# Kernel optimization log

Measured on AMD Instinct MI355X. Metric: run time of the kernel, lower is better.

The kernel has to match this reference:

```python
import jax, jax.numpy as jnp
import numpy as np

B, C, H, I = 32, 8, 512, 512


def act(x):
    # CustomActivation == hardtanh: (|x+1| - |x-1|) / 2
    return (jnp.abs(x + 1.0) - jnp.abs(x - 1.0)) * 0.5


def setup_inputs() -> dict:
    key = jax.random.key(0)
    ks = jax.random.split(key, 12)
    inp = jax.random.normal(ks[0], (B, C, H, I), dtype=jnp.float32)
    p_mask = jax.random.normal(ks[1], (H, I), dtype=jnp.float32)
    # Wp: tril(randn) with diagonal filled to 1 (matches __init__ + the no_grad
    # tril/clamp projection in forward, which is a no-op right after init).
    Wp = jnp.tril(jax.random.normal(ks[2], (H, H), dtype=jnp.float32))
    Wp = Wp - jnp.diag(jnp.diag(Wp)) + jnp.eye(H, dtype=jnp.float32)
    Wp_diag = jnp.ones((H,), dtype=jnp.float32)
    Wzp = jax.random.normal(ks[3], (H, H), dtype=jnp.float32)
    s = 1.0 / np.sqrt(I)
    def lin(k):
        kw, kb = jax.random.split(k)
        W = jax.random.uniform(kw, (I, I), jnp.float32, -s, s)
        b = jax.random.uniform(kb, (I,), jnp.float32, -s, s)
        return W, b
    p_lin_w, p_lin_b = lin(ks[4])
    z_lin_w, z_lin_b = lin(ks[5])
    fc1_w, fc1_b = lin(ks[6])
    fc2_w, fc2_b = lin(ks[7])
    return {
        'input': inp, 'p_mask': p_mask, 'Wp': Wp, 'Wp_diag': Wp_diag, 'Wzp': Wzp,
        'p_lin_w': p_lin_w, 'p_lin_b': p_lin_b,
        'z_lin_w': z_lin_w, 'z_lin_b': z_lin_b,
        'fc1_w': fc1_w, 'fc1_b': fc1_b, 'fc2_w': fc2_w, 'fc2_b': fc2_b,
    }


def reference(input, p_mask, Wp, Wp_diag, Wzp,
              p_lin_w, p_lin_b, z_lin_w, z_lin_b,
              fc1_w, fc1_b, fc2_w, fc2_b):
    x = input * (1.0 / 5000.0)                      # [B,C,H,I]
    p_set = x * act(p_mask)                         # split_input, broadcast over B,C
    Wp_eff = Wp + jnp.diag(Wp_diag)                 # [H,H]
    # per-channel Wp @ p_set[c], batched over B and C in one GEMM
    tp = jnp.einsum('hk,bcki->bchi', Wp_eff, p_set)
    tp = act(act(tp) @ p_lin_w.T + p_lin_b)         # p_output_layer
    tz = jnp.einsum('hk,bchi->bchi', Wzp, tp)       # wait-free channel-batched GEMM
    tz = act(act(tz) @ z_lin_w.T + z_lin_b)         # z_output_layer
    # sum over in_channel (out_channel==1 so broadcast-accumulate == sum)
    combined = tp.sum(axis=1) + tz.sum(axis=1) + x[:, 0]  # [B,H,I]
    out = jax.nn.relu(combined @ fc1_w.T + fc1_b)
    out = out @ fc2_w.T + fc2_b
    return out
```

## Files before the change

kernel.cpp:

```cpp
#include <hip/hip_runtime.h>

namespace {

constexpr int Bn = 32, Cn = 8, Hn = 512, In = 512;
constexpr size_t HI = (size_t)Hn * In;
constexpr float SC = 1.0f / 5000.0f;

using s16x8 = __attribute__((ext_vector_type(8))) short;
using f32x4 = __attribute__((ext_vector_type(4))) float;

__device__ __forceinline__ float actf(float x) {
    return fminf(1.0f, fmaxf(-1.0f, x));
}

__device__ __forceinline__ unsigned short f2bf(float f) {
    unsigned u = __builtin_bit_cast(unsigned, f);
    u += 0x7FFFu + ((u >> 16) & 1u);
    return (unsigned short)(u >> 16);
}
__device__ __forceinline__ float bf2f(unsigned short h) {
    return __builtin_bit_cast(float, (unsigned)h << 16);
}

__device__ __forceinline__ void async16(const void* g, void* l) {
    __builtin_amdgcn_global_load_lds(
        (const __attribute__((address_space(1))) unsigned*)g,
        (__attribute__((address_space(3))) unsigned*)l, 16, 0, 0);
}

#define CFENCE asm volatile("" ::: "memory")
#define BAR do { CFENCE; __builtin_amdgcn_s_barrier(); CFENCE; } while (0)

template<int EPI, bool PCOL, bool TRI>
__global__ __launch_bounds__(512, 2) void gemm256_8p(
    const unsigned short* __restrict__ A,
    const unsigned short* __restrict__ Bt,
    const float* __restrict__ bias,
    const float* __restrict__ zrow,
    unsigned short* __restrict__ out0,
    unsigned short* __restrict__ out1,
    size_t sB, size_t sC)
{
    __shared__ __align__(16) char lds[131072];
    char* daA = lds;
    char* dbA = lds + 32768;
    char* daB = lds + 65536;
    char* dbB = lds + 98304;

    const int tid = threadIdx.x;
    const int lane = tid & 63, l15 = lane & 15, kq = lane >> 4;
    const int wid = tid >> 6, wm = wid >> 2, wn = wid & 3;

    const int bid = blockIdx.x;
    int rt, ct; size_t zb;
    if (PCOL) {
        const int p = ((bid >> 5) << 3) | (bid & 7);
        const int q = (bid >> 3) & 3;
        zb = (size_t)p; rt = q >> 1; ct = q & 1;
    } else {
        const int p = ((bid >> 4) << 3) | (bid & 7);
        const int q = (bid >> 3) & 1;
        zb = 0; rt = p; ct = q;
    }

    const char* Ab = (const char*)A + (size_t)rt * 256 * 1024;
    const char* Bb = (const char*)(Bt + zb * sB) + (size_t)ct * 256 * 1024;

    const int nkt = TRI ? (rt + 1) * 4 : 8;
    const int nit = nkt >> 1;

    const int srow8 = tid >> 3;
    const int csw   = ((tid & 7) ^ (srow8 & 7)) << 4;

    auto stageH = [&](const char* src, int kt, int half, char* dstTile) {
        const char* s = src + ((size_t)half * 128 + srow8) * 1024 + kt * 128 + csw;
        char* d = dstTile + half * 16384 + tid * 16;
        async16(s,             d);
        async16(s + 64 * 1024, d + 8192);
    };

    const int kx0 = ((kq    ) ^ (l15 & 7)) << 4;
    const int kx1 = ((kq + 4) ^ (l15 & 7)) << 4;

    auto rdA4 = [&](const char* tile, int mlo, s16x8 a[2][4]) {
        #pragma unroll
        for (int i = 0; i < 4; ++i) {
            const int row = wm * 128 + (mlo + i) * 16 + l15;
            a[0][i] = *(const s16x8*)(tile + row * 128 + kx0);
            a[1][i] = *(const s16x8*)(tile + row * 128 + kx1);
        }
    };
    auto rdB2 = [&](const char* tile, int nlo, s16x8 b[2][2]) {
        #pragma unroll
        for (int j = 0; j < 2; ++j) {
            const int row = wn * 64 + (nlo + j) * 16 + l15;
            b[0][j] = *(const s16x8*)(tile + row * 128 + kx0);
            b[1][j] = *(const s16x8*)(tile + row * 128 + kx1);
        }
    };

    f32x4 acc[8][4] = {};

    auto QMM = [&](s16x8 a[2][4], s16x8 b[2][2], int mlo, int nlo) {
        __builtin_amdgcn_s_setprio(1);
        #pragma unroll
        for (int kk = 0; kk < 2; ++kk)
            #pragma unroll
            for (int i = 0; i < 4; ++i)
                #pragma unroll
                for (int j = 0; j < 2; ++j)
                    acc[mlo + i][nlo + j] = __builtin_amdgcn_mfma_f32_16x16x32_bf16(
                        a[kk][i], b[kk][j], acc[mlo + i][nlo + j], 0, 0, 0);
        __builtin_amdgcn_s_setprio(0);
    };

    stageH(Bb, 0, 0, daB); stageH(Bb, 0, 1, daB);
    stageH(Ab, 0, 0, daA); stageH(Ab, 0, 1, daA);
    stageH(Bb, 1, 0, dbB); stageH(Bb, 1, 1, dbB);
    asm volatile("s_waitcnt vmcnt(4)" ::: "memory");
    BAR;

    #pragma unroll 1
    for (int t = 0; t < nit; ++t) {
        const int j = 2 * t;
        const bool more = (t + 1 < nit);
        s16x8 a03[2][4], a47[2][4], b01[2][2], b23[2][2];

        rdA4(daA, 0, a03); rdB2(daB, 0, b01);
        stageH(Ab, j + 1, 0, dbA);
        BAR; QMM(a03, b01, 0, 0); BAR;
        rdB2(daB, 2, b23);
        stageH(Ab, j + 1, 1, dbA);
        BAR; QMM(a03, b23, 0, 2); BAR;
        rdA4(daA, 4, a47);
        if (more) stageH(Bb, j + 2, 0, daB);
        BAR; QMM(a47, b23, 4, 2); BAR;
        if (more) stageH(Bb, j + 2, 1, daB);
        BAR; QMM(a47, b01, 4, 0);
        if (more) asm volatile("s_waitcnt vmcnt(4)" ::: "memory");
        else      asm volatile("s_waitcnt vmcnt(0)" ::: "memory");
        BAR;

        rdA4(dbA, 0, a03); rdB2(dbB, 0, b01);
        if (more) stageH(Ab, j + 2, 0, daA);
        BAR; QMM(a03, b01, 0, 0); BAR;
        rdB2(dbB, 2, b23);
        if (more) stageH(Ab, j + 2, 1, daA);
        BAR; QMM(a03, b23, 0, 2); BAR;
        rdA4(dbA, 4, a47);
        if (more) stageH(Bb, j + 3, 0, dbB);
        BAR; QMM(a47, b23, 4, 2); BAR;
        if (more) stageH(Bb, j + 3, 1, dbB);
        BAR; QMM(a47, b01, 4, 0);
        if (more) { asm volatile("s_waitcnt vmcnt(4)" ::: "memory"); BAR; }
        else BAR;
    }

    const int rbase = rt * 256 + wm * 128 + kq * 4;
    const int cb    = ct * 256 + wn * 64 + l15;
    #pragma unroll
    for (int mi = 0; mi < 8; ++mi) {
        #pragma unroll
        for (int n = 0; n < 4; ++n) {
            const int c = cb + n * 16;
            const float bs = (EPI == 0) ? 0.0f : bias[c];
            #pragma unroll
            for (int jj = 0; jj < 4; ++jj) {
                const size_t r = (size_t)rbase + mi * 16 + jj;
                const size_t idx = zb * sC + r * 512 + c;
                float v = acc[mi][n][jj];
                if (EPI == 0) {
                    out0[idx] = f2bf(actf(v));
                } else if (EPI == 1) {
                    float tp = actf(v + bs);
                    out0[idx] = f2bf(tp);
                    out1[idx] = f2bf(actf(zrow[r & 511] * tp));
                } else {
                    out0[idx] = f2bf(actf(v + bs));
                }
            }
        }
    }
}

template<int EPI>
__global__ __launch_bounds__(256, 3) void mfma_gemm128(
    const unsigned short* __restrict__ A,
    const unsigned short* __restrict__ Bt,
    const float* __restrict__ bias,
    unsigned short* __restrict__ out0,
    float* __restrict__ outf)
{
    __shared__ __align__(16) char lds[2][16384];

    const int tid  = threadIdx.x;
    const int wid  = tid >> 6, lane = tid & 63;
    const int wr   = wid >> 1, wc = wid & 1;
    const int l15  = lane & 15, kq = lane >> 4;

    const int bid = blockIdx.x;
    const int p = ((bid >> 5) << 3) | (bid & 7);
    const int q = (bid >> 3) & 3;
    const int rt = p, ct = q;

    const char* Ab = (const char*)A + (size_t)rt * 131072;
    const char* Bb = (const char*)Bt + (size_t)ct * 131072;

    f32x4 acc[4][4] = {};

    const int o0  = tid * 16;
    const int r0s = o0 >> 6;
    const int c0s = o0 & 63;
    const int csw = c0s ^ (((r0s >> 1) & 3) << 4);

    auto stage = [&](char* buf, int k0b) {
        async16(Ab + (size_t)r0s * 1024 + k0b + csw,        buf + wid * 1024);
        async16(Ab + (size_t)(64 + r0s) * 1024 + k0b + csw, buf + 4096 + wid * 1024);
        async16(Bb + (size_t)r0s * 1024 + k0b + csw,        buf + 8192 + wid * 1024);
        async16(Bb + (size_t)(64 + r0s) * 1024 + k0b + csw, buf + 12288 + wid * 1024);
    };
    auto compute = [&](const char* buf) {
        s16x8 a[4], b[4];
        const int kx = kq * 16 ^ (((l15 >> 1) & 3) << 4);
        const int ar = wr * 64 + l15;
        const int br = wc * 64 + l15;
        #pragma unroll
        for (int m = 0; m < 4; ++m)
            a[m] = *(const s16x8*)(buf + (size_t)(ar + m * 16) * 64 + kx);
        #pragma unroll
        for (int n = 0; n < 4; ++n)
            b[n] = *(const s16x8*)(buf + 8192 + (size_t)(br + n * 16) * 64 + kx);
        #pragma unroll
        for (int m = 0; m < 4; ++m)
            #pragma unroll
            for (int n = 0; n < 4; ++n)
                acc[m][n] = __builtin_amdgcn_mfma_f32_16x16x32_bf16(a[m], b[n], acc[m][n], 0, 0, 0);
    };

    stage(lds[0], 0);
    stage(lds[1], 64);

    #pragma unroll 1
    for (int ks = 0; ks < 16; ks += 2) {
        const bool more = (ks + 2 < 16);
        asm volatile("s_waitcnt vmcnt(4)" ::: "memory");
        BAR;
        compute(lds[0]);
        BAR;
        if (more) stage(lds[0], (ks + 2) * 64);
        if (more) asm volatile("s_waitcnt vmcnt(4)" ::: "memory");
        else      asm volatile("s_waitcnt vmcnt(0)" ::: "memory");
        BAR;
        compute(lds[1]);
        BAR;
        if (more) stage(lds[1], (ks + 3) * 64);
    }

    const int cb = ct * 128 + wc * 64 + l15;
    const int rb = rt * 128 + wr * 64 + (kq << 2);
    #pragma unroll
    for (int m = 0; m < 4; ++m)
        #pragma unroll
        for (int n = 0; n < 4; ++n) {
            const int c = cb + n * 16;
            #pragma unroll
            for (int j = 0; j < 4; ++j) {
                const int r = rb + m * 16 + j;
                const size_t idx = (size_t)r * 512 + c;
                float v = acc[m][n][j] + bias[c];
                if (EPI == 3) out0[idx] = f2bf(fmaxf(v, 0.0f));
                else          outf[idx] = v;
            }
        }
}

__global__ __launch_bounds__(256) void reduce_both(
    const unsigned short* __restrict__ tp,
    const unsigned short* __restrict__ tz,
    const float* __restrict__ x0,
    unsigned short* __restrict__ comb)
{
    size_t idx = (size_t)blockIdx.x * 256 + threadIdx.x;
    size_t b = idx >> 16;
    size_t p = (idx & 65535) * 4;
    float4 xv = *(const float4*)&x0[(b * Cn) * HI + p];
    float s0 = xv.x * SC, s1 = xv.y * SC, s2 = xv.z * SC, s3 = xv.w * SC;
    #pragma unroll
    for (int c = 0; c < Cn; ++c) {
        size_t q = (b * Cn + c) * HI + p;
        ushort4 a = *(const ushort4*)&tp[q];
        ushort4 d = *(const ushort4*)&tz[q];
        s0 += bf2f(a.x) + bf2f(d.x);
        s1 += bf2f(a.y) + bf2f(d.y);
        s2 += bf2f(a.z) + bf2f(d.z);
        s3 += bf2f(a.w) + bf2f(d.w);
    }
    ushort4 o;
    o.x = f2bf(s0); o.y = f2bf(s1); o.z = f2bf(s2); o.w = f2bf(s3);
    *(ushort4*)&comb[b * HI + p] = o;
}

__global__ __launch_bounds__(256) void transpose_mask(
    const float* __restrict__ x, const float* __restrict__ mask,
    unsigned short* __restrict__ xst)
{
    __shared__ float t[64][65];
    const int bc = blockIdx.z;
    const int i0 = blockIdx.x * 64, k0 = blockIdx.y * 64;
    const int r4 = threadIdx.x >> 6, cc = threadIdx.x & 63;
    const float* xp = x + (size_t)bc * HI;
    #pragma unroll
    for (int it = 0; it < 16; ++it) {
        int kl = it * 4 + r4;
        size_t g = (size_t)(k0 + kl) * In + i0 + cc;
        t[kl][cc] = xp[g] * (actf(mask[g]) * SC);
    }
    __syncthreads();
    unsigned short* op = xst + (size_t)bc * HI;
    #pragma unroll
    for (int it = 0; it < 16; ++it) {
        int il = it * 4 + r4;
        op[(size_t)(i0 + il) * Hn + k0 + cc] = f2bf(t[cc][il]);
    }
}

__global__ __launch_bounds__(256) void prep_wpe_bf(
    const float* __restrict__ Wp, const float* __restrict__ Wpd,
    unsigned short* __restrict__ o)
{
    int idx = blockIdx.x * 256 + threadIdx.x;
    int i = idx >> 9, j = idx & 511;
    o[idx] = f2bf(Wp[idx] + (i == j ? Wpd[i] : 0.0f));
}

__global__ __launch_bounds__(256) void conv_bf(
    const float* __restrict__ s, unsigned short* __restrict__ o)
{
    int idx = blockIdx.x * 256 + threadIdx.x;
    o[idx] = f2bf(s[idx]);
}

__global__ __launch_bounds__(64) void rowsum(
    const float* __restrict__ W, float* __restrict__ zr)
{
    int h = blockIdx.x, l = threadIdx.x;
    float s = 0.0f;
    for (int k = l; k < Hn; k += 64) s += W[h * Hn + k];
    #pragma unroll
    for (int off = 32; off; off >>= 1) s += __shfl_down(s, off, 64);
    if (!l) zr[h] = s;
}

}

extern "C" void kernel_launch(void* const* d_in, const int* in_sizes, int n_in,
                              void* d_out, int out_size, void* d_ws, size_t ws_size,
                              hipStream_t stream)
{
    const float* input  = (const float*)d_in[0];
    const float* p_mask = (const float*)d_in[1];
    const float* Wp     = (const float*)d_in[2];
    const float* Wpd    = (const float*)d_in[3];
    const float* Wzp    = (const float*)d_in[4];
    const float* plw    = (const float*)d_in[5];
    const float* plb    = (const float*)d_in[6];
    const float* zlw    = (const float*)d_in[7];
    const float* zlb    = (const float*)d_in[8];
    const float* f1w    = (const float*)d_in[9];
    const float* f1b    = (const float*)d_in[10];
    const float* f2w    = (const float*)d_in[11];
    const float* f2b    = (const float*)d_in[12];

    constexpr size_t WB = 512 * 512 * 2;
    char* w = (char*)d_ws;
    auto alloc = [&](size_t bytes) { char* p = w; w += (bytes + 255) & ~255ull; return p; };

    unsigned short* Wpeb  = (unsigned short*)alloc(WB);
    unsigned short* plwb  = (unsigned short*)alloc(WB);
    unsigned short* zlwb  = (unsigned short*)alloc(WB);
    unsigned short* f1wb  = (unsigned short*)alloc(WB);
    unsigned short* f2wb  = (unsigned short*)alloc(WB);
    float*          zrw   = (float*)alloc(512 * 4);
    unsigned short* combb = (unsigned short*)alloc((size_t)Bn * HI * 2);
    unsigned short* out1  = (unsigned short*)alloc((size_t)Bn * HI * 2);

    size_t fixedB = (size_t)(w - (char*)d_ws);
    int chunk = 32;
    while (chunk > 1 &&
           fixedB + 4ull * (size_t)chunk * Cn * HI * 2 + 4096 > ws_size)
        chunk >>= 1;
    const size_t CB = (size_t)chunk * Cn * HI * 2;
    unsigned short* xst   = (unsigned short*)alloc(CB);
    unsigned short* tpact = (unsigned short*)alloc(CB);
    unsigned short* tpb   = (unsigned short*)alloc(CB);
    unsigned short* tzin  = (unsigned short*)alloc(CB);
    unsigned short* tzb   = xst;

    prep_wpe_bf<<<512 * 512 / 256, 256, 0, stream>>>(Wp, Wpd, Wpeb);
    conv_bf<<<1024, 256, 0, stream>>>(plw, plwb);
    conv_bf<<<1024, 256, 0, stream>>>(zlw, zlwb);
    conv_bf<<<1024, 256, 0, stream>>>(f1w, f1wb);
    conv_bf<<<1024, 256, 0, stream>>>(f2w, f2wb);
    rowsum<<<512, 64, 0, stream>>>(Wzp, zrw);

    for (int b0 = 0; b0 < Bn; b0 += chunk) {
        const int nc = chunk * Cn;
        const float* inp_c = input + (size_t)b0 * Cn * HI;

        transpose_mask<<<dim3(8, 8, nc), 256, 0, stream>>>(inp_c, p_mask, xst);
        gemm256_8p<0, true, true><<<nc * 4, 512, 0, stream>>>(
            Wpeb, xst, nullptr, nullptr, tpact, nullptr, HI, HI);
        gemm256_8p<1, false, false><<<nc * 4, 512, 0, stream>>>(
            tpact, plwb, plb, zrw, tpb, tzin, 0, 0);
        gemm256_8p<2, false, false><<<nc * 4, 512, 0, stream>>>(
            tzin, zlwb, zlb, nullptr, tzb, nullptr, 0, 0);
        reduce_both<<<chunk * 256, 256, 0, stream>>>(
            tpb, tzb, inp_c, combb + (size_t)b0 * HI);
    }

    mfma_gemm128<3><<<512, 256, 0, stream>>>(combb, f1wb, f1b, out1, nullptr);
    mfma_gemm128<4><<<512, 256, 0, stream>>>(out1, f2wb, f2b, nullptr, (float*)d_out);
}
```

Before: 489.5 us.

## Vectorize memory-bound helper kernels, fuse weight conversions, reorder triangular tiles

The reduce kernel now handles 8 elements per thread with 16-byte loads and stores, and its grid is halved to match. The transpose/mask kernel reads inputs as float4 and writes ushort4. The four weight bf16 conversions are merged into a single vectorized launch. In the triangular GEMM, the row-tile order is flipped so the heavier lower row tile is scheduled first, which should even out load imbalance. Each change is meant to cut memory instruction count or launch overhead. The transpose now does strided LDS reads with column access, which could raise bank conflicts.

Result: no change. 489.2 us, median of 2 (-0.1%).

```diff
diff --git a/kernel.cpp b/kernel.cpp
--- a/kernel.cpp
+++ b/kernel.cpp
@@ -7,6 +7,7 @@
 constexpr float SC = 1.0f / 5000.0f;
 
 using s16x8 = __attribute__((ext_vector_type(8))) short;
+using u16x8 = __attribute__((ext_vector_type(8))) unsigned short;
 using f32x4 = __attribute__((ext_vector_type(4))) float;
 
 __device__ __forceinline__ float actf(float x) {
@@ -56,7 +57,7 @@
     if (PCOL) {
         const int p = ((bid >> 5) << 3) | (bid & 7);
         const int q = (bid >> 3) & 3;
-        zb = (size_t)p; rt = q >> 1; ct = q & 1;
+        zb = (size_t)p; rt = 1 - (q >> 1); ct = q & 1;
     } else {
         const int p = ((bid >> 4) << 3) | (bid & 7);
         const int q = (bid >> 3) & 1;
@@ -281,23 +282,24 @@
     unsigned short* __restrict__ comb)
 {
     size_t idx = (size_t)blockIdx.x * 256 + threadIdx.x;
-    size_t b = idx >> 16;
-    size_t p = (idx & 65535) * 4;
-    float4 xv = *(const float4*)&x0[(b * Cn) * HI + p];
-    float s0 = xv.x * SC, s1 = xv.y * SC, s2 = xv.z * SC, s3 = xv.w * SC;
+    size_t b = idx >> 15;
+    size_t p = (idx & 32767) * 8;
+    float4 xa = *(const float4*)&x0[(b * Cn) * HI + p];
+    float4 xb = *(const float4*)&x0[(b * Cn) * HI + p + 4];
+    float s[8] = { xa.x * SC, xa.y * SC, xa.z * SC, xa.w * SC,
+                   xb.x * SC, xb.y * SC, xb.z * SC, xb.w * SC };
     #pragma unroll
     for (int c = 0; c < Cn; ++c) {
         size_t q = (b * Cn + c) * HI + p;
-        ushort4 a = *(const ushort4*)&tp[q];
-        ushort4 d = *(const ushort4*)&tz[q];
-        s0 += bf2f(a.x) + bf2f(d.x);
-        s1 += bf2f(a.y) + bf2f(d.y);
-        s2 += bf2f(a.z) + bf2f(d.z);
-        s3 += bf2f(a.w) + bf2f(d.w);
-    }
-    ushort4 o;
-    o.x = f2bf(s0); o.y = f2bf(s1); o.z = f2bf(s2); o.w = f2bf(s3);
-    *(ushort4*)&comb[b * HI + p] = o;
+        u16x8 a = *(const u16x8*)&tp[q];
+        u16x8 d = *(const u16x8*)&tz[q];
+        #pragma unroll
+        for (int j = 0; j < 8; ++j) s[j] += bf2f(a[j]) + bf2f(d[j]);
+    }
+    u16x8 o;
+    #pragma unroll
+    for (int j = 0; j < 8; ++j) o[j] = f2bf(s[j]);
+    *(u16x8*)&comb[b * HI + p] = o;
 }
 
 __global__ __launch_bounds__(256) void transpose_mask(
@@ -307,20 +309,31 @@
     __shared__ float t[64][65];
     const int bc = blockIdx.z;
     const int i0 = blockIdx.x * 64, k0 = blockIdx.y * 64;
-    const int r4 = threadIdx.x >> 6, cc = threadIdx.x & 63;
+    const int r16 = threadIdx.x >> 4;
+    const int c4  = (threadIdx.x & 15) * 4;
     const float* xp = x + (size_t)bc * HI;
     #pragma unroll
-    for (int it = 0; it < 16; ++it) {
-        int kl = it * 4 + r4;
-        size_t g = (size_t)(k0 + kl) * In + i0 + cc;
-        t[kl][cc] = xp[g] * (actf(mask[g]) * SC);
+    for (int ps = 0; ps < 4; ++ps) {
+        const int kl = ps * 16 + r16;
+        const size_t g = (size_t)(k0 + kl) * In + i0 + c4;
+        float4 xv = *(const float4*)&xp[g];
+        float4 mv = *(const float4*)&mask[g];
+        t[kl][c4 + 0] = xv.x * (actf(mv.x) * SC);
+        t[kl][c4 + 1] = xv.y * (actf(mv.y) * SC);
+        t[kl][c4 + 2] = xv.z * (actf(mv.z) * SC);
+        t[kl][c4 + 3] = xv.w * (actf(mv.w) * SC);
     }
     __syncthreads();
     unsigned short* op = xst + (size_t)bc * HI;
     #pragma unroll
-    for (int it = 0; it < 16; ++it) {
-        int il = it * 4 + r4;
-        op[(size_t)(i0 + il) * Hn + k0 + cc] = f2bf(t[cc][il]);
+    for (int ps = 0; ps < 4; ++ps) {
+        const int il = ps * 16 + r16;
+        ushort4 o;
+        o.x = f2bf(t[c4 + 0][il]);
+        o.y = f2bf(t[c4 + 1][il]);
+        o.z = f2bf(t[c4 + 2][il]);
+        o.w = f2bf(t[c4 + 3][il]);
+        *(ushort4*)&op[(size_t)(i0 + il) * Hn + k0 + c4] = o;
     }
 }
 
@@ -333,11 +346,20 @@
     o[idx] = f2bf(Wp[idx] + (i == j ? Wpd[i] : 0.0f));
 }
 
-__global__ __launch_bounds__(256) void conv_bf(
-    const float* __restrict__ s, unsigned short* __restrict__ o)
-{
-    int idx = blockIdx.x * 256 + threadIdx.x;
-    o[idx] = f2bf(s[idx]);
+__global__ __launch_bounds__(256) void conv_bf4(
+    const float* __restrict__ s0, const float* __restrict__ s1,
+    const float* __restrict__ s2, const float* __restrict__ s3,
+    unsigned short* __restrict__ d0, unsigned short* __restrict__ d1,
+    unsigned short* __restrict__ d2, unsigned short* __restrict__ d3)
+{
+    const int m = blockIdx.x >> 8;
+    const int idx = ((blockIdx.x & 255) * 256 + threadIdx.x);
+    const float* s = (m == 0) ? s0 : (m == 1) ? s1 : (m == 2) ? s2 : s3;
+    unsigned short* d = (m == 0) ? d0 : (m == 1) ? d1 : (m == 2) ? d2 : d3;
+    float4 v = ((const float4*)s)[idx];
+    ushort4 o;
+    o.x = f2bf(v.x); o.y = f2bf(v.y); o.z = f2bf(v.z); o.w = f2bf(v.w);
+    ((ushort4*)d)[idx] = o;
 }
 
 __global__ __launch_bounds__(64) void rowsum(
@@ -397,10 +419,7 @@
     unsigned short* tzb   = xst;
 
     prep_wpe_bf<<<512 * 512 / 256, 256, 0, stream>>>(Wp, Wpd, Wpeb);
-    conv_bf<<<1024, 256, 0, stream>>>(plw, plwb);
-    conv_bf<<<1024, 256, 0, stream>>>(zlw, zlwb);
-    conv_bf<<<1024, 256, 0, stream>>>(f1w, f1wb);
-    conv_bf<<<1024, 256, 0, stream>>>(f2w, f2wb);
+    conv_bf4<<<1024, 256, 0, stream>>>(plw, zlw, f1w, f2w, plwb, zlwb, f1wb, f2wb);
     rowsum<<<512, 64, 0, stream>>>(Wzp, zrw);
 
     for (int b0 = 0; b0 < Bn; b0 += chunk) {
@@ -414,7 +433,7 @@
             tpact, plwb, plb, zrw, tpb, tzin, 0, 0);
         gemm256_8p<2, false, false><<<nc * 4, 512, 0, stream>>>(
             tzin, zlwb, zlb, nullptr, tzb, nullptr, 0, 0);
-        reduce_both<<<chunk * 256, 256, 0, stream>>>(
+        reduce_both<<<chunk * 128, 256, 0, stream>>>(
             tpb, tzb, inp_c, combb + (size_t)b0 * HI);
     }
 
```
